# Performance work log

Hardware: AMD Instinct MI355X
Metric: run time of the kernel (lower is better)

The kernel has to match this reference:

```python
import jax, jax.numpy as jnp
import numpy as np

B, C, S, H, W = 8, 8, 16, 48, 48
N = H * W
MIN_SCALE, MAX_SCALE = 1.0, 100.0


def setup_inputs() -> dict:
    key = jax.random.key(0)
    x = jax.random.normal(key, (B, C, H, W), dtype=jnp.float32)
    # learned parameter: scales = linspace(min_scale, max_scale, num_scales)
    scales = jnp.linspace(MIN_SCALE, MAX_SCALE, S, dtype=jnp.float32)
    return {"x": x, "scales": scales, "i": 0}


def _wavelets(scales, n):
    # Ricker-like wavelet evaluated on t = 0..n-1 (NOT centered, as in the original)
    # f = 1/scale, sigma = 1/(2*pi*f) = scale/(2*pi)
    t = jnp.arange(n, dtype=scales.dtype)            # [N]
    sigma = scales / (2.0 * jnp.pi)                  # [S]
    t2 = t[None, :] ** 2                             # [1, N]
    s2 = sigma[:, None] ** 2                         # [S, 1]
    return (1.0 - t2 / s2) * jnp.exp(-t2 / (2.0 * s2))  # [S, N]


def reference(x, scales, i):
    b, c = x.shape[0], x.shape[1]
    n = x.shape[2] * x.shape[3]
    s = scales.shape[0]
    xf = x.reshape(b, c, n)                          # [B, C, N]
    wav = _wavelets(scales, n)                       # [S, N]
    # torch: stack per-scale wavelets then .repeat(fdim,1,1) -> kernel k uses scale k % S
    w = jnp.tile(wav, (c, 1))[:, None, :]            # [C*S, 1, N]
    # torch: x.repeat(1, S, 1) -> channel k uses input channel k % C
    xr = jnp.tile(xf, (1, s, 1))                     # [B, S*C, N]
    # F.conv1d(padding='same') with kernel length n: total pad n-1, extra on the right
    total = n - 1
    left = total // 2
    out = jax.lax.conv_general_dilated(
        xr, w,
        window_strides=(1,),
        padding=((left, total - left),),
        dimension_numbers=("NCH", "OIH", "NCH"),
        feature_group_count=c * s)                   # [B, C*S, N]
    return out
```

## Files before the change

kernel.cpp:

```cpp
#include <hip/hip_runtime.h>


#define NPIX 2304
#define NC 8
#define LEFT 1151
#define TILE 1152
#define THREADS 576
#define JCAP 512

__global__ __launch_bounds__(THREADS)
void wavelet_conv_kernel(const float* __restrict__ x,
                         const float* __restrict__ scales,
                         float* __restrict__ out) {
    __shared__ float ws[JCAP];
    __shared__ float xp[TILE + JCAP];

    const int bx   = blockIdx.x;
    const int pair = bx >> 1;
    const int half = bx & 1;
    const int b    = pair >> 4;
    const int d    = pair & 15;
    const int c    = d & 7;
    const int t0   = half * TILE;
    const int tid  = threadIdx.x;

    const float scale  = scales[d];
    const float sigma  = scale * 0.15915494309189535f;
    const float inv_s2 = 1.0f / (sigma * sigma);
    int jmax = (int)(12.0f * sigma) + 4;
    if (jmax > NPIX) jmax = NPIX;
    if (jmax > JCAP) jmax = JCAP;

    for (int i = tid; i < jmax; i += THREADS) {
        float fj = (float)i;
        float a  = fj * fj * inv_s2;
        ws[i] = (1.0f - a) * __expf(-0.5f * a);
    }
    const float* xrow = x + (size_t)(b * NC + c) * NPIX;
    const int xlen = TILE + jmax;
    for (int i = tid; i < xlen; i += THREADS) {
        int g = t0 - LEFT + i;
        xp[i] = (g >= 0 && g < NPIX) ? xrow[g] : 0.0f;
    }
    __syncthreads();

    const int base = 2 * tid;
    float acc0 = 0.0f, acc1 = 0.0f;
    float xc = xp[base];
    #pragma unroll 4
    for (int j = 0; j < jmax; ++j) {
        float wv = ws[j];
        float xn = xp[base + j + 1];
        acc0 = fmaf(xc, wv, acc0);
        acc1 = fmaf(xn, wv, acc1);
        xc = xn;
    }

    const int n0 = t0 + base;
    float2 v = make_float2(acc0, acc1);
    #pragma unroll
    for (int kk = 0; kk < 8; ++kk) {
        int k = d + 16 * kk;
        *reinterpret_cast<float2*>(out + (size_t)(b * 128 + k) * NPIX + n0) = v;
    }
}

extern "C" void kernel_launch(void* const* d_in, const int* in_sizes, int n_in,
                              void* d_out, int out_size, void* d_ws, size_t ws_size,
                              hipStream_t stream) {
    const float* x      = (const float*)d_in[0];
    const float* scales = (const float*)d_in[1];
    float* out          = (float*)d_out;
    wavelet_conv_kernel<<<256, THREADS, 0, stream>>>(x, scales, out);
}
```

Before: 12.15 us.

## Register-block four outputs per thread with float4 LDS loads and stores

Each thread now computes four adjacent outputs instead of two, reading the input window and wavelet taps as float4 from shared memory. This cuts LDS reads per FMA and widens the output stores to float4. The tile shrinks to 768 pixels with 192 threads over 384 blocks. The tap count is padded to a multiple of four and the shared input buffer grows to match. The trade-off is fewer threads per block and more register pressure.

```diff
diff --git a/kernel.cpp b/kernel.cpp
--- a/kernel.cpp
+++ b/kernel.cpp
@@ -4,8 +4,8 @@
 #define NPIX 2304
 #define NC 8
 #define LEFT 1151
-#define TILE 1152
-#define THREADS 576
+#define TILE 768
+#define THREADS 192
 #define JCAP 512
 
 __global__ __launch_bounds__(THREADS)
@@ -13,55 +13,72 @@
                          const float* __restrict__ scales,
                          float* __restrict__ out) {
     __shared__ float ws[JCAP];
-    __shared__ float xp[TILE + JCAP];
+    __shared__ float xp[TILE + JCAP + 4];
 
     const int bx   = blockIdx.x;
-    const int pair = bx >> 1;
-    const int half = bx & 1;
+    const int pair = bx / 3;
+    const int tile = bx - 3 * pair;
     const int b    = pair >> 4;
     const int d    = pair & 15;
     const int c    = d & 7;
-    const int t0   = half * TILE;
+    const int t0   = tile * TILE;
     const int tid  = threadIdx.x;
 
     const float scale  = scales[d];
     const float sigma  = scale * 0.15915494309189535f;
     const float inv_s2 = 1.0f / (sigma * sigma);
     int jmax = (int)(12.0f * sigma) + 4;
-    if (jmax > NPIX) jmax = NPIX;
-    if (jmax > JCAP) jmax = JCAP;
+    if (jmax > JCAP - 4) jmax = JCAP - 4;
+    const int jpad = (jmax + 3) & ~3;
+    const int gmax = jpad >> 2;
 
-    for (int i = tid; i < jmax; i += THREADS) {
+    for (int i = tid; i < jpad; i += THREADS) {
         float fj = (float)i;
         float a  = fj * fj * inv_s2;
         ws[i] = (1.0f - a) * __expf(-0.5f * a);
     }
     const float* xrow = x + (size_t)(b * NC + c) * NPIX;
-    const int xlen = TILE + jmax;
+    const int xlen = TILE + jpad + 4;
     for (int i = tid; i < xlen; i += THREADS) {
         int g = t0 - LEFT + i;
         xp[i] = (g >= 0 && g < NPIX) ? xrow[g] : 0.0f;
     }
     __syncthreads();
 
-    const int base = 2 * tid;
-    float acc0 = 0.0f, acc1 = 0.0f;
-    float xc = xp[base];
-    #pragma unroll 4
-    for (int j = 0; j < jmax; ++j) {
-        float wv = ws[j];
-        float xn = xp[base + j + 1];
-        acc0 = fmaf(xc, wv, acc0);
-        acc1 = fmaf(xn, wv, acc1);
-        xc = xn;
+    const int base = 4 * tid;
+    const float4* xp4 = reinterpret_cast<const float4*>(xp + base);
+    const float4* ws4 = reinterpret_cast<const float4*>(ws);
+    float a0 = 0.f, a1 = 0.f, a2 = 0.f, a3 = 0.f;
+    float4 xa = xp4[0];
+    #pragma unroll 2
+    for (int g = 0; g < gmax; ++g) {
+        float4 xb = xp4[g + 1];
+        float4 wq = ws4[g];
+        a0 = fmaf(xa.x, wq.x, a0);
+        a1 = fmaf(xa.y, wq.x, a1);
+        a2 = fmaf(xa.z, wq.x, a2);
+        a3 = fmaf(xa.w, wq.x, a3);
+        a0 = fmaf(xa.y, wq.y, a0);
+        a1 = fmaf(xa.z, wq.y, a1);
+        a2 = fmaf(xa.w, wq.y, a2);
+        a3 = fmaf(xb.x, wq.y, a3);
+        a0 = fmaf(xa.z, wq.z, a0);
+        a1 = fmaf(xa.w, wq.z, a1);
+        a2 = fmaf(xb.x, wq.z, a2);
+        a3 = fmaf(xb.y, wq.z, a3);
+        a0 = fmaf(xa.w, wq.w, a0);
+        a1 = fmaf(xb.x, wq.w, a1);
+        a2 = fmaf(xb.y, wq.w, a2);
+        a3 = fmaf(xb.z, wq.w, a3);
+        xa = xb;
     }
 
     const int n0 = t0 + base;
-    float2 v = make_float2(acc0, acc1);
+    float4 v = make_float4(a0, a1, a2, a3);
     #pragma unroll
     for (int kk = 0; kk < 8; ++kk) {
         int k = d + 16 * kk;
-        *reinterpret_cast<float2*>(out + (size_t)(b * 128 + k) * NPIX + n0) = v;
+        *reinterpret_cast<float4*>(out + (size_t)(b * 128 + k) * NPIX + n0) = v;
     }
 }
 
@@ -71,5 +88,5 @@
     const float* x      = (const float*)d_in[0];
     const float* scales = (const float*)d_in[1];
     float* out          = (float*)d_out;
-    wavelet_conv_kernel<<<256, THREADS, 0, stream>>>(x, scales, out);
+    wavelet_conv_kernel<<<384, THREADS, 0, stream>>>(x, scales, out);
 }
```

New measurement: 13.30 us. 1.09x slower.
